# Kernel tuning notes

Hardware: AMD Instinct MI355X
Metric: run time of the kernel (lower is better)

The kernel has to match this reference:

```python
import jax, jax.numpy as jnp
import numpy as np

N_FEATURES = 256
HIDDEN = 16
BATCH = 32768


def setup_inputs() -> dict:
    key = jax.random.key(0)
    ks = jax.random.split(key, 8)
    F, H = N_FEATURES, HIDDEN
    x = jax.random.normal(ks[0], (BATCH, F), dtype=jnp.float32)
    # Stacked per-feature subnet params (torch Linear: y = x @ W.T + b)
    s1 = 1.0  # fan_in=1 for fc1
    W1 = jax.random.uniform(ks[1], (F, H), minval=-s1, maxval=s1, dtype=jnp.float32)
    b1 = jax.random.uniform(ks[2], (F, H), minval=-s1, maxval=s1, dtype=jnp.float32)
    s2 = 1.0 / np.sqrt(H)
    W2 = jax.random.uniform(ks[3], (F, H, H), minval=-s2, maxval=s2, dtype=jnp.float32)  # [F, out, in]
    b2 = jax.random.uniform(ks[4], (F, H), minval=-s2, maxval=s2, dtype=jnp.float32)
    W3 = jax.random.uniform(ks[5], (F, H), minval=-s2, maxval=s2, dtype=jnp.float32)  # out=1
    b3 = jax.random.uniform(ks[6], (F,), minval=-s2, maxval=s2, dtype=jnp.float32)
    linear_a = jnp.zeros((F,), dtype=jnp.float32)
    bias_b = jnp.zeros((1,), dtype=jnp.float32)
    return {"x": x, "linear_a": linear_a, "bias_b": bias_b,
            "W1": W1, "b1": b1, "W2": W2, "b2": b2, "W3": W3, "b3": b3}


def reference(x, linear_a, bias_b, W1, b1, W2, b2, W3, b3):
    # lin term: (x * a).sum(1)
    lin = x @ linear_a  # [B]
    # all subnets batched: h1 [B, F, H]
    h1 = jax.nn.relu(x[:, :, None] * W1[None, :, :] + b1[None, :, :])
    # fc2: y = h1 @ W2.T per feature; W2 is [F, out, in]
    h2 = jax.nn.relu(jnp.einsum('bfh,fkh->bfk', h1, W2) + b2[None, :, :])
    # fc3 -> scalar per feature, then sum over features
    out_f = jnp.einsum('bfh,fh->bf', h2, W3) + b3[None, :]  # [B, F]
    add_sum = out_f.sum(axis=1)  # [B]
    logits = lin + bias_b[0] + add_sum
    return logits
```

## Files before the change

### kernel.cpp

```cpp
#include <hip/hip_runtime.h>


typedef float    f32x4 __attribute__((ext_vector_type(4)));
typedef _Float16 f16x4 __attribute__((ext_vector_type(4)));
typedef __fp16   pk16x2 __attribute__((ext_vector_type(2)));

__device__ __forceinline__ f16x4 cvt4(f32x4 v) {
    pk16x2 lo = __builtin_amdgcn_cvt_pkrtz(v[0], v[1]);
    pk16x2 hi = __builtin_amdgcn_cvt_pkrtz(v[2], v[3]);
    union { unsigned u[2]; f16x4 h; } un;
    un.u[0] = __builtin_bit_cast(unsigned, lo);
    un.u[1] = __builtin_bit_cast(unsigned, hi);
    return un.h;
}

__device__ __forceinline__ f16x4 splat_h(float s) {
    pk16x2 p = __builtin_amdgcn_cvt_pkrtz(s, s);
    unsigned u = __builtin_bit_cast(unsigned, p);
    union { unsigned u[2]; f16x4 h; } un;
    un.u[0] = u; un.u[1] = u;
    return un.h;
}

__device__ __forceinline__ f16x4 relu_h(f16x4 v) {
    f16x4 z = {};
    return __builtin_elementwise_max(v, z);
}

__device__ __forceinline__ f32x4 relu_f(f32x4 v) {
    f32x4 z = {0.f, 0.f, 0.f, 0.f};
    return __builtin_elementwise_max(v, z);
}

#define FCHUNK 16
#define LDSR   18

__global__ __launch_bounds__(256, 7) void igann_kernel(
    const float* __restrict__ x,  const float* __restrict__ la,
    const float* __restrict__ bb, const float* __restrict__ W1,
    const float* __restrict__ b1, const float* __restrict__ W2,
    const float* __restrict__ b2, const float* __restrict__ W3,
    const float* __restrict__ b3, float* __restrict__ out)
{
    const int tid = threadIdx.x;
    const int l   = tid & 63;
    const int w   = tid >> 6;
    const int r   = l & 15;
    const int g   = l >> 4;
    const int g4  = g * 4;
    const int r16 = r * 16;

    const int rb = blockIdx.x >> 4;
    const int fg = blockIdx.x & 15;
    const int f0 = fg * FCHUNK;
    const int rowbase = rb * 256;

    __shared__ float ldsx[256 * LDSR];
    __shared__ float red[256];

    {
        const int rr = tid >> 2;
        const int c4 = (tid & 3) * 4;
        #pragma unroll
        for (int it = 0; it < 4; ++it) {
            const int row = it * 64 + rr;
            f32x4 v = *(const f32x4*)(x + (size_t)(rowbase + row) * 256 + f0 + c4);
            *(f32x4*)(ldsx + row * LDSR + c4) = v;
        }
    }
    __syncthreads();

    const float* xw = ldsx + (w * 64 + r) * LDSR;

    f32x4 acc[4];
    #pragma unroll
    for (int t = 0; t < 4; ++t) acc[t] = (f32x4){0.f, 0.f, 0.f, 0.f};

    for (int fi = 0; fi < FCHUNK; fi += 4) {
        f32x4 xv[4];
        #pragma unroll
        for (int t = 0; t < 4; ++t)
            xv[t] = *(const f32x4*)(xw + t * 16 * LDSR + fi);

        #pragma unroll
        for (int u = 0; u < 4; ++u) {
            const int f = f0 + fi + u;
            f16x4 w1h = cvt4(*(const f32x4*)(W1 + f * 16 + g4));
            f16x4 b1h = cvt4(*(const f32x4*)(b1 + f * 16 + g4));
            f16x4 bfrag = cvt4(*(const f32x4*)(W2 + (size_t)f * 256 + r16 + g4));
            const float b2k = b2[f * 16 + r];
            const float w3k = W3[f * 16 + r];
            const f32x4 cinit = {b2k, b2k, b2k, b2k};
            const f32x4 w3k4  = {w3k, w3k, w3k, w3k};

            #pragma unroll
            for (int t = 0; t < 4; ++t) {
                f16x4 xs4 = splat_h(xv[t][u]);
                f16x4 h = relu_h(xs4 * w1h + b1h);
                f32x4 d = __builtin_amdgcn_mfma_f32_16x16x16f16(h, bfrag, cinit, 0, 0, 0);
                acc[t] += relu_f(d) * w3k4;
            }
        }
    }

    #pragma unroll
    for (int t = 0; t < 4; ++t)
        #pragma unroll
        for (int j = 0; j < 4; ++j) {
            float v = acc[t][j];
            v += __shfl_xor(v, 1, 64);
            v += __shfl_xor(v, 2, 64);
            v += __shfl_xor(v, 4, 64);
            v += __shfl_xor(v, 8, 64);
            if (r == 0) red[w * 64 + t * 16 + g4 + j] = v;
        }
    __syncthreads();

    float lin = 0.f, b3s = 0.f;
    const float* xrow = ldsx + tid * LDSR;
    #pragma unroll
    for (int c = 0; c < 16; ++c) {
        lin = fmaf(xrow[c], la[f0 + c], lin);
        b3s += b3[f0 + c];
    }
    const float v = red[tid] + lin + b3s + (fg == 0 ? bb[0] : 0.f);
    atomicAdd(out + rowbase + tid, v);
}

extern "C" void kernel_launch(void* const* d_in, const int* in_sizes, int n_in,
                              void* d_out, int out_size, void* d_ws, size_t ws_size,
                              hipStream_t stream) {
    const float* x  = (const float*)d_in[0];
    const float* la = (const float*)d_in[1];
    const float* bb = (const float*)d_in[2];
    const float* W1 = (const float*)d_in[3];
    const float* b1 = (const float*)d_in[4];
    const float* W2 = (const float*)d_in[5];
    const float* b2 = (const float*)d_in[6];
    const float* W3 = (const float*)d_in[7];
    const float* b3 = (const float*)d_in[8];
    float* out = (float*)d_out;

    (void)hipMemsetAsync(out, 0, (size_t)out_size * sizeof(float), stream);

    dim3 grid(2048), block(256);
    hipLaunchKernelGGL(igann_kernel, grid, block, 0, stream,
                       x, la, bb, W1, b1, W2, b2, W3, b3, out);
}
```

Measured before the change: 130.1 us.

## Stage per-feature weights in LDS as fp16 and store x tile as fp16

Each block now loads its W2, W1, b1, b2 and W3 slices into shared memory once, converting to fp16 up front. Previously every wave re-read them from global memory and converted them inside the inner loop. The x tile is also stored as fp16 in LDS, which removes the per-element splat conversion and halves LDS footprint for x. The feature loop is fully unrolled, and launch bounds occupancy drops from 7 to 6 to make room. The linear term now reads x in fp16, which adds a small precision loss.

```diff
diff --git a/kernel.cpp b/kernel.cpp
--- a/kernel.cpp
+++ b/kernel.cpp
@@ -14,14 +14,6 @@
     return un.h;
 }
 
-__device__ __forceinline__ f16x4 splat_h(float s) {
-    pk16x2 p = __builtin_amdgcn_cvt_pkrtz(s, s);
-    unsigned u = __builtin_bit_cast(unsigned, p);
-    union { unsigned u[2]; f16x4 h; } un;
-    un.u[0] = u; un.u[1] = u;
-    return un.h;
-}
-
 __device__ __forceinline__ f16x4 relu_h(f16x4 v) {
     f16x4 z = {};
     return __builtin_elementwise_max(v, z);
@@ -33,9 +25,10 @@
 }
 
 #define FCHUNK 16
-#define LDSR   18
+#define XR     20
+#define W2R    20
 
-__global__ __launch_bounds__(256, 7) void igann_kernel(
+__global__ __launch_bounds__(256, 6) void igann_kernel(
     const float* __restrict__ x,  const float* __restrict__ la,
     const float* __restrict__ bb, const float* __restrict__ W1,
     const float* __restrict__ b1, const float* __restrict__ W2,
@@ -48,15 +41,19 @@
     const int r   = l & 15;
     const int g   = l >> 4;
     const int g4  = g * 4;
-    const int r16 = r * 16;
 
     const int rb = blockIdx.x >> 4;
     const int fg = blockIdx.x & 15;
     const int f0 = fg * FCHUNK;
     const int rowbase = rb * 256;
 
-    __shared__ float ldsx[256 * LDSR];
-    __shared__ float red[256];
+    __shared__ _Float16 xs [256 * XR];
+    __shared__ _Float16 w2s[FCHUNK * 16 * W2R];
+    __shared__ _Float16 w1s[FCHUNK * 16];
+    __shared__ _Float16 b1s[FCHUNK * 16];
+    __shared__ float    b2s[FCHUNK * 16];
+    __shared__ float    w3s[FCHUNK * 16];
+    __shared__ float    red[256];
 
     {
         const int rr = tid >> 2;
@@ -65,38 +62,54 @@
         for (int it = 0; it < 4; ++it) {
             const int row = it * 64 + rr;
             f32x4 v = *(const f32x4*)(x + (size_t)(rowbase + row) * 256 + f0 + c4);
-            *(f32x4*)(ldsx + row * LDSR + c4) = v;
+            *(f16x4*)(xs + row * XR + c4) = cvt4(v);
         }
     }
+    {
+        const int f = tid >> 4, n = tid & 15;
+        const float* src = W2 + ((size_t)(f0 + f) * 16 + n) * 16;
+        _Float16* dst = w2s + (f * 16 + n) * W2R;
+        #pragma unroll
+        for (int q = 0; q < 4; ++q) {
+            f32x4 v = *(const f32x4*)(src + q * 4);
+            *(f16x4*)(dst + q * 4) = cvt4(v);
+        }
+    }
+    w1s[tid] = (_Float16)W1[f0 * 16 + tid];
+    b1s[tid] = (_Float16)b1[f0 * 16 + tid];
+    b2s[tid] = b2[f0 * 16 + tid];
+    w3s[tid] = W3[f0 * 16 + tid];
     __syncthreads();
 
-    const float* xw = ldsx + (w * 64 + r) * LDSR;
+    const _Float16* xw = xs + (w * 64 + r) * XR;
 
     f32x4 acc[4];
     #pragma unroll
     for (int t = 0; t < 4; ++t) acc[t] = (f32x4){0.f, 0.f, 0.f, 0.f};
 
+    #pragma unroll
     for (int fi = 0; fi < FCHUNK; fi += 4) {
-        f32x4 xv[4];
+        f16x4 xv[4];
         #pragma unroll
         for (int t = 0; t < 4; ++t)
-            xv[t] = *(const f32x4*)(xw + t * 16 * LDSR + fi);
+            xv[t] = *(const f16x4*)(xw + t * 16 * XR + fi);
 
         #pragma unroll
         for (int u = 0; u < 4; ++u) {
-            const int f = f0 + fi + u;
-            f16x4 w1h = cvt4(*(const f32x4*)(W1 + f * 16 + g4));
-            f16x4 b1h = cvt4(*(const f32x4*)(b1 + f * 16 + g4));
-            f16x4 bfrag = cvt4(*(const f32x4*)(W2 + (size_t)f * 256 + r16 + g4));
-            const float b2k = b2[f * 16 + r];
-            const float w3k = W3[f * 16 + r];
+            const int f = fi + u;
+            f16x4 w1h   = *(const f16x4*)(w1s + f * 16 + g4);
+            f16x4 b1h   = *(const f16x4*)(b1s + f * 16 + g4);
+            f16x4 bfrag = *(const f16x4*)(w2s + (f * 16 + r) * W2R + g4);
+            const float b2k = b2s[f * 16 + r];
+            const float w3k = w3s[f * 16 + r];
             const f32x4 cinit = {b2k, b2k, b2k, b2k};
             const f32x4 w3k4  = {w3k, w3k, w3k, w3k};
 
             #pragma unroll
             for (int t = 0; t < 4; ++t) {
-                f16x4 xs4 = splat_h(xv[t][u]);
-                f16x4 h = relu_h(xs4 * w1h + b1h);
+                const _Float16 s = xv[t][u];
+                f16x4 xb = {s, s, s, s};
+                f16x4 h = relu_h(xb * w1h + b1h);
                 f32x4 d = __builtin_amdgcn_mfma_f32_16x16x16f16(h, bfrag, cinit, 0, 0, 0);
                 acc[t] += relu_f(d) * w3k4;
             }
@@ -117,10 +130,10 @@
     __syncthreads();
 
     float lin = 0.f, b3s = 0.f;
-    const float* xrow = ldsx + tid * LDSR;
+    const _Float16* xrow = xs + tid * XR;
     #pragma unroll
-    for (int c = 0; c < 16; ++c) {
-        lin = fmaf(xrow[c], la[f0 + c], lin);
+    for (int c = 0; c < FCHUNK; ++c) {
+        lin = fmaf((float)xrow[c], la[f0 + c], lin);
         b3s += b3[f0 + c];
     }
     const float v = red[tid] + lin + b3s + (fg == 0 ? bb[0] : 0.f);
```

After: 233.1 us. 79.2% more time.
